# Optimization experiments

Measured on AMD Instinct MI355X. Metric: run time of the kernel, lower is better.

Reference implementation:

```python
import jax, jax.numpy as jnp
import numpy as np

B, C, OUTC, H, W, K, P, S = 4, 64, 64, 128, 128, 3, 1, 1
KK = K * K


def setup_inputs() -> dict:
    key = jax.random.key(0)
    ks = jax.random.split(key, 5)
    x = jax.random.normal(ks[0], (B, C, H, W), dtype=jnp.float32)
    # small-scale offset weights keep learned offsets in a realistic few-pixel range
    w_off = jax.random.normal(ks[1], (2 * KK, C, 3, 3), dtype=jnp.float32) * 0.05
    b_off = jnp.zeros((2 * KK,), dtype=jnp.float32)
    w_mask = jax.random.normal(ks[2], (KK, C, 3, 3), dtype=jnp.float32) * 0.05
    b_mask = jnp.zeros((KK,), dtype=jnp.float32)
    w_dcn = jax.random.normal(ks[3], (OUTC, C, K, K), dtype=jnp.float32) * (1.0 / np.sqrt(C * KK))
    b_dcn = jnp.zeros((OUTC,), dtype=jnp.float32)
    return {"x": x, "w_off": w_off, "b_off": b_off, "w_mask": w_mask,
            "b_mask": b_mask, "w_dcn": w_dcn, "b_dcn": b_dcn}


def _conv3x3(x, w, b):
    y = jax.lax.conv_general_dilated(x, w, (1, 1), ((1, 1), (1, 1)),
                                     dimension_numbers=("NCHW", "OIHW", "NCHW"))
    return y + b[None, :, None, None]


def _deform_conv(x, offset, mask, w, b):
    # torchvision DeformConv2d (v2, modulated). offset layout: [B, kk, (dy,dx), H, W]
    Ho = (H + 2 * P - K) // S + 1
    Wo = (W + 2 * P - K) // S + 1
    off = offset.reshape(B, KK, 2, Ho, Wo)
    dy, dx = off[:, :, 0], off[:, :, 1]                      # [B,kk,Ho,Wo]
    ki, kj = jnp.meshgrid(jnp.arange(K), jnp.arange(K), indexing="ij")
    ki = ki.reshape(KK).astype(jnp.float32)
    kj = kj.reshape(KK).astype(jnp.float32)
    hg = (jnp.arange(Ho) * S - P).astype(jnp.float32)
    wg = (jnp.arange(Wo) * S - P).astype(jnp.float32)
    py = dy + ki[None, :, None, None] + hg[None, None, :, None]   # sample y coord
    px = dx + kj[None, :, None, None] + wg[None, None, None, :]   # sample x coord

    y0f = jnp.floor(py)
    x0f = jnp.floor(px)
    ly = py - y0f
    lx = px - x0f
    y0 = y0f.astype(jnp.int32)
    x0 = x0f.astype(jnp.int32)

    x_flat = x.reshape(B, C, H * W)

    def sample(yi, xi, wgt):
        valid = (yi >= 0) & (yi < H) & (xi >= 0) & (xi < W)
        idx = jnp.clip(yi, 0, H - 1) * W + jnp.clip(xi, 0, W - 1)  # [B,kk,Ho,Wo]
        g = jax.vmap(lambda xb, ib: xb[:, ib])(x_flat, idx)        # [B,C,kk,Ho,Wo]
        return g * (wgt * valid)[:, None]

    acc = (sample(y0, x0, (1 - ly) * (1 - lx))
           + sample(y0, x0 + 1, (1 - ly) * lx)
           + sample(y0 + 1, x0, ly * (1 - lx))
           + sample(y0 + 1, x0 + 1, ly * lx))                      # [B,C,kk,Ho,Wo]
    acc = acc * mask.reshape(B, 1, KK, Ho, Wo)
    out = jnp.einsum("bckhw,ock->bohw", acc, w.reshape(OUTC, C, KK))
    return out + b[None, :, None, None]


def reference(x, w_off, b_off, w_mask, b_mask, w_dcn, b_dcn):
    offset = _conv3x3(x, w_off, b_off)
    mask = jax.nn.sigmoid(_conv3x3(x, w_mask, b_mask))
    out = _deform_conv(x, offset, mask, w_dcn, b_dcn)
    return out, offset
```

## Files before the change

kernel.cpp:

```cpp
#include <hip/hip_runtime.h>
#include <hip/hip_bf16.h>
#include <math.h>

#define BB 4
#define CC 64
#define OCN 64
#define HH 128
#define WW 128
#define HW (HH*WW)
#define KKN 9
#define APAD 200

typedef short short8 __attribute__((ext_vector_type(8)));
typedef short short4v __attribute__((ext_vector_type(4)));
typedef float floatx4 __attribute__((ext_vector_type(4)));
typedef unsigned int uintx4 __attribute__((ext_vector_type(4)));

__device__ __forceinline__ float bf2f_us(unsigned short u) {
    return __uint_as_float(((unsigned)u) << 16);
}
__device__ __forceinline__ short f2bfs(float f) {
    __hip_bfloat16 h = __float2bfloat16(f);
    return *reinterpret_cast<short*>(&h);
}
__device__ __forceinline__ uintx4 as_u4(short8 v) {
    union { short8 s; uintx4 u; } x; x.s = v; return x.u;
}
__device__ __forceinline__ float blo(unsigned d) { return __uint_as_float(d << 16); }
__device__ __forceinline__ float bhi(unsigned d) { return __uint_as_float(d & 0xffff0000u); }

__global__ __launch_bounds__(256) void transpose_prep(
    const float* __restrict__ x,
    const float* __restrict__ w_dcn, const float* __restrict__ w_off,
    const float* __restrict__ b_off, const float* __restrict__ w_mask,
    const float* __restrict__ b_mask,
    __hip_bfloat16* __restrict__ xt, __hip_bfloat16* __restrict__ wTf,
    __hip_bfloat16* __restrict__ wOf, float* __restrict__ rebias)
{
    int blk = blockIdx.x;
    int tid = threadIdx.x;
    if (blk < BB * 512) {
        __shared__ float tile[64][33];
        int pixbase = (blk & 511) * 32;
        int b       = blk >> 9;
        const float* xb = x + (size_t)b * CC * HW;
        int p = tid & 31;
        #pragma unroll
        for (int i = 0; i < 8; ++i) {
            int c = (tid >> 5) * 8 + i;
            tile[c][p] = xb[(size_t)c * HW + pixbase + p];
        }
        __syncthreads();
        __hip_bfloat16* xo = xt + ((size_t)b * HW + pixbase) * CC;
        int pixl = tid >> 3;
        int c8t  = tid & 7;
        short8 o;
        #pragma unroll
        for (int i = 0; i < 8; ++i) o[i] = f2bfs(tile[c8t * 8 + i][pixl]);
        *reinterpret_cast<short8*>(&xo[(size_t)pixl * CC + c8t * 8]) = o;
        return;
    }
    int i = (blk - BB * 512) * 256 + tid;
    if (i < 18 * 4 * 64 * 8) {
        int jj = i & 7;
        int l  = (i >> 3) & 63;
        int nt = (i >> 9) & 3;
        int s  = i >> 11;
        int oc = nt * 16 + (l & 15);
        int kk = s * 32 + ((l >> 4) << 3) + jj;
        int c  = kk & 63;
        int kt = kk >> 6;
        wTf[i] = __float2bfloat16(w_dcn[(oc * CC + c) * 9 + kt]);
    }
    int j = i - 18 * 4 * 64 * 8;
    if (j >= 0 && j < 18 * 2 * 64 * 8) {
        int jj = j & 7;
        int l  = (j >> 3) & 63;
        int nt = (j >> 9) & 1;
        int s  = j >> 10;
        int oc = nt * 16 + (l & 15);
        int kk = s * 32 + ((l >> 4) << 3) + jj;
        int c  = kk & 63;
        int kt = kk >> 6;
        float v = 0.0f;
        if (oc < 18)      v = w_off[(oc * CC + c) * 9 + kt];
        else if (oc < 27) v = w_mask[((oc - 18) * CC + c) * 9 + kt];
        wOf[j] = __float2bfloat16(v);
    }
    int r = j - 18 * 2 * 64 * 8;
    if (r >= 0 && r < 27) rebias[r] = (r < 18) ? b_off[r] : b_mask[r - 18];
}

__global__ __launch_bounds__(256, 4) void deform_fused(
    const __hip_bfloat16* __restrict__ xt,
    const __hip_bfloat16* __restrict__ wTf, const __hip_bfloat16* __restrict__ wOf,
    const float* __restrict__ rebias, const float* __restrict__ b_dcn,
    float* __restrict__ off_out, float* __restrict__ out)
{
    __shared__ __align__(16) __hip_bfloat16 accs[64][APAD];
    __shared__ uintx4 tabs[KKN][64];
    __shared__ __hip_bfloat16 offs_l[18][68];
    __shared__ __hip_bfloat16 ms_l[KKN][68];

    int tid    = threadIdx.x;
    int lane   = tid & 63;
    int wv     = __builtin_amdgcn_readfirstlane(tid >> 6);
    int lane15 = lane & 15;
    int lq     = lane >> 4;
    int nt     = wv & 1;
    int ph     = wv >> 1;
    int pix    = tid >> 3;
    int c8     = tid & 7;
    int co     = c8 * 16;
    int kreg   = lq << 3;

    int wo0 = (blockIdx.x & 1) * 64;
    int row = (blockIdx.x >> 1) & (HH - 1);
    int b   = blockIdx.x >> 8;

    const char* xtb = (const char*)(xt + (size_t)b * HW * CC);
    const short8* wTf8 = (const short8*)wTf;
    const short8* wOf8 = (const short8*)wOf;
    const short8 zero8 = {0,0,0,0,0,0,0,0};

    floatx4 accomA[2] = {{0,0,0,0},{0,0,0,0}};
    for (int chunk = 0; chunk < 3; ++chunk) {
        int y = row + chunk - 1;
        bool yvalid = (unsigned)y < (unsigned)HH;
        int yc = min(max(y, 0), HH - 1);
        short8 v[2][3];
        #pragma unroll
        for (int h = 0; h < 2; ++h) {
            #pragma unroll
            for (int kl = 0; kl < 3; ++kl) {
                int xw = wo0 + h * 32 + pix + kl - 1;
                bool valid = yvalid && ((unsigned)xw < (unsigned)WW);
                int xc = min(max(xw, 0), WW - 1);
                short8 t = *(const short8*)(xtb + (((yc * WW) + xc) << 7) + co);
                v[h][kl] = valid ? t : zero8;
            }
        }
        #pragma unroll
        for (int h = 0; h < 2; ++h)
            #pragma unroll
            for (int kl = 0; kl < 3; ++kl)
                *reinterpret_cast<short8*>(&accs[h * 32 + pix][kl * 64 + c8 * 8]) = v[h][kl];
        __syncthreads();

        #pragma unroll
        for (int step = 0; step < 6; ++step) {
            int s = chunk * 6 + step;
            short8 bfrag = wOf8[(size_t)(s * 2 + nt) * 64 + lane];
            #pragma unroll
            for (int q = 0; q < 2; ++q) {
                int pg = ph * 2 + q;
                short8 a = *reinterpret_cast<const short8*>(&accs[pg * 16 + lane15][step * 32 + kreg]);
                accomA[q] = __builtin_amdgcn_mfma_f32_16x16x32_bf16(a, bfrag, accomA[q], 0, 0, 0);
            }
        }
        __syncthreads();
    }

    #pragma unroll
    for (int q = 0; q < 2; ++q) {
        int pg = ph * 2 + q;
        int pcl = pg * 16 + lq * 4;
        int oc = nt * 16 + lane15;
        if (oc < 18) {
            float bias = rebias[oc];
            floatx4 o = accomA[q];
            o[0] += bias; o[1] += bias; o[2] += bias; o[3] += bias;
            *reinterpret_cast<floatx4*>(
                &off_out[(((size_t)b * 18 + oc) * HH + row) * WW + wo0 + pcl]) = o;
            short4v ob = { f2bfs(o[0]), f2bfs(o[1]), f2bfs(o[2]), f2bfs(o[3]) };
            *reinterpret_cast<short4v*>(&offs_l[oc][pcl]) = ob;
        } else if (oc < 27) {
            float bias = rebias[oc];
            short4v mb;
            #pragma unroll
            for (int t = 0; t < 4; ++t)
                mb[t] = f2bfs(1.0f / (1.0f + expf(-(accomA[q][t] + bias))));
            *reinterpret_cast<short4v*>(&ms_l[oc - 18][pcl]) = mb;
        }
    }
    __syncthreads();

    for (int e = tid; e < KKN * 64; e += 256) {
        int k = e >> 6, p = e & 63;
        float dy = bf2f_us(*(const unsigned short*)&offs_l[2 * k][p]);
        float dx = bf2f_us(*(const unsigned short*)&offs_l[2 * k + 1][p]);
        float m  = bf2f_us(*(const unsigned short*)&ms_l[k][p]);
        float py = dy + (float)(k / 3) + (float)(row - 1);
        float px = dx + (float)(k % 3) + (float)(wo0 + p - 1);
        float y0f = floorf(py), x0f = floorf(px);
        float ly = py - y0f, lx = px - x0f;
        int y0 = (int)y0f, x0 = (int)x0f;
        uintx4 rec;
        #pragma unroll
        for (int t = 0; t < 4; ++t) {
            int yi = y0 + (t >> 1), xi = x0 + (t & 1);
            float wy = (t >> 1) ? ly : 1.0f - ly;
            float wx = (t & 1)  ? lx : 1.0f - lx;
            bool valid = ((unsigned)yi < (unsigned)HH) && ((unsigned)xi < (unsigned)WW);
            int yc2 = min(max(yi, 0), HH - 1);
            int xc2 = min(max(xi, 0), WW - 1);
            __hip_bfloat16 hw = __float2bfloat16(valid ? wy * wx * m : 0.0f);
            unsigned short wb = *reinterpret_cast<unsigned short*>(&hw);
            rec[t] = (unsigned)(yc2 * WW + xc2) | ((unsigned)wb << 16);
        }
        tabs[k][p] = rec;
    }
    __syncthreads();

    short8 buf[2][4];
    uintx4 tb[2];
    floatx4 accv[4] = {{0,0,0,0},{0,0,0,0},{0,0,0,0},{0,0,0,0}};

#define ISSUE(G) do { \
    uintx4 _t = tabs[(G) >> 1][pix + ((G) & 1) * 32]; \
    tb[(G) & 1] = _t; \
    buf[(G) & 1][0] = *(const short8*)(xtb + ((_t[0] & 0xffffu) << 7) + co); \
    buf[(G) & 1][1] = *(const short8*)(xtb + ((_t[1] & 0xffffu) << 7) + co); \
    buf[(G) & 1][2] = *(const short8*)(xtb + ((_t[2] & 0xffffu) << 7) + co); \
    buf[(G) & 1][3] = *(const short8*)(xtb + ((_t[3] & 0xffffu) << 7) + co); \
} while (0)

#define COMBINE(G) do { \
    float fA[8] = {0,0,0,0,0,0,0,0}; \
    _Pragma("unroll") \
    for (int t = 0; t < 4; ++t) { \
        float wt = __uint_as_float(tb[(G) & 1][t] & 0xffff0000u); \
        uintx4 dA = as_u4(buf[(G) & 1][t]); \
        _Pragma("unroll") \
        for (int jq = 0; jq < 4; ++jq) { \
            fA[2 * jq]     = fmaf(wt, blo(dA[jq]), fA[2 * jq]); \
            fA[2 * jq + 1] = fmaf(wt, bhi(dA[jq]), fA[2 * jq + 1]); \
        } \
    } \
    short8 oA; \
    _Pragma("unroll") \
    for (int jq = 0; jq < 8; ++jq) { oA[jq] = f2bfs(fA[jq]); } \
    *reinterpret_cast<short8*>( \
        &accs[((G) & 1) * 32 + pix][(((G) >> 1) % 3) * 64 + c8 * 8]) = oA; \
} while (0)

#define CMFMA(CH) do { \
    _Pragma("unroll") \
    for (int step = 0; step < 6; ++step) { \
        int s = (CH) * 6 + step; \
        short8 bfrag = wTf8[(size_t)(s * 4 + wv) * 64 + lane]; \
        _Pragma("unroll") \
        for (int pg = 0; pg < 4; ++pg) { \
            short8 a = *reinterpret_cast<const short8*>(&accs[pg * 16 + lane15][step * 32 + kreg]); \
            accv[pg] = __builtin_amdgcn_mfma_f32_16x16x32_bf16(a, bfrag, accv[pg], 0, 0, 0); \
        } \
    } \
} while (0)

    ISSUE(0); ISSUE(1);
    COMBINE(0); ISSUE(2);
    COMBINE(1); ISSUE(3);
    COMBINE(2); ISSUE(4);
    COMBINE(3); ISSUE(5);
    COMBINE(4); COMBINE(5);
    __syncthreads();
    ISSUE(6); ISSUE(7);
    CMFMA(0);
    asm volatile("s_waitcnt lgkmcnt(0)" ::: "memory");
    __builtin_amdgcn_s_barrier();
    COMBINE(6); ISSUE(8);
    COMBINE(7); ISSUE(9);
    COMBINE(8); ISSUE(10);
    COMBINE(9); ISSUE(11);
    COMBINE(10); COMBINE(11);
    __syncthreads();
    ISSUE(12); ISSUE(13);
    CMFMA(1);
    asm volatile("s_waitcnt lgkmcnt(0)" ::: "memory");
    __builtin_amdgcn_s_barrier();
    COMBINE(12); ISSUE(14);
    COMBINE(13); ISSUE(15);
    COMBINE(14); ISSUE(16);
    COMBINE(15); ISSUE(17);
    COMBINE(16); COMBINE(17);
    __syncthreads();
    CMFMA(2);

#undef ISSUE
#undef COMBINE
#undef CMFMA

    {
        int oc = wv * 16 + lane15;
        float bias = b_dcn[oc];
        #pragma unroll
        for (int pg = 0; pg < 4; ++pg) {
            int pcol = wo0 + pg * 16 + lq * 4;
            floatx4 o = accv[pg];
            o[0] += bias; o[1] += bias; o[2] += bias; o[3] += bias;
            *reinterpret_cast<floatx4*>(&out[(((size_t)b * OCN + oc) * HH + row) * WW + pcol]) = o;
        }
    }
}

extern "C" void kernel_launch(void* const* d_in, const int* in_sizes, int n_in,
                              void* d_out, int out_size, void* d_ws, size_t ws_size,
                              hipStream_t stream) {
    const float* x      = (const float*)d_in[0];
    const float* w_off  = (const float*)d_in[1];
    const float* b_off  = (const float*)d_in[2];
    const float* w_mask = (const float*)d_in[3];
    const float* b_mask = (const float*)d_in[4];
    const float* w_dcn  = (const float*)d_in[5];
    const float* b_dcn  = (const float*)d_in[6];

    float* out     = (float*)d_out;
    float* off_out = out + (size_t)BB * OCN * HW;

    float* rebias  = (float*)d_ws;
    __hip_bfloat16* xt  = (__hip_bfloat16*)(rebias + 32);
    __hip_bfloat16* wTf = xt + (size_t)BB * HW * CC;
    __hip_bfloat16* wOf = wTf + 18 * 4 * 64 * 8;

    int prep_total  = 18 * 4 * 64 * 8 + 18 * 2 * 64 * 8 + 27;
    int prep_blocks = (prep_total + 255) / 256;
    transpose_prep<<<BB * 512 + prep_blocks, 256, 0, stream>>>(
        x, w_dcn, w_off, b_off, w_mask, b_mask, xt, wTf, wOf, rebias);

    deform_fused<<<BB * HH * 2, 256, 0, stream>>>(
        xt, wTf, wOf, rebias, b_dcn, off_out, out);
}
```

Baseline: 39.96 us.

## Overhaul transpose, offset-conv loads, gather pipelining and block order in deform kernel

The transpose prep kernel now handles 64 pixels per block, reading with float4 loads into an XOR-swizzled shared tile so the transposed reads avoid bank conflicts. The offset/mask conv loads its MFMA A fragments straight from global memory into registers, which removes the LDS staging and two barriers per row chunk. The deformable gather pipeline goes from double to triple buffering so three gathers are in flight before each combine, and the combine uses packed float2 FMAs. Block indices are swizzled so neighbouring blocks land on different rows, which may change cache locality. The cost is more registers, which could reduce occupancy, and redundant global loads in the offset conv.

```diff
diff --git a/kernel.cpp b/kernel.cpp
--- a/kernel.cpp
+++ b/kernel.cpp
@@ -14,6 +14,7 @@
 typedef short short8 __attribute__((ext_vector_type(8)));
 typedef short short4v __attribute__((ext_vector_type(4)));
 typedef float floatx4 __attribute__((ext_vector_type(4)));
+typedef float floatx2 __attribute__((ext_vector_type(2)));
 typedef unsigned int uintx4 __attribute__((ext_vector_type(4)));
 
 __device__ __forceinline__ float bf2f_us(unsigned short u) {
@@ -39,28 +40,34 @@
 {
     int blk = blockIdx.x;
     int tid = threadIdx.x;
-    if (blk < BB * 512) {
-        __shared__ float tile[64][33];
-        int pixbase = (blk & 511) * 32;
-        int b       = blk >> 9;
+    if (blk < BB * 256) {
+        __shared__ float tile[64][64];
+        int pixbase = (blk & 255) * 64;
+        int b       = blk >> 8;
         const float* xb = x + (size_t)b * CC * HW;
-        int p = tid & 31;
-        #pragma unroll
-        for (int i = 0; i < 8; ++i) {
-            int c = (tid >> 5) * 8 + i;
-            tile[c][p] = xb[(size_t)c * HW + pixbase + p];
+        #pragma unroll
+        for (int i = 0; i < 4; ++i) {
+            int c  = (tid >> 4) + i * 16;
+            int p4 = (tid & 15) * 4;
+            floatx4 v = *reinterpret_cast<const floatx4*>(xb + (size_t)c * HW + pixbase + p4);
+            int cs = p4 ^ (((c >> 3) & 7) << 2);
+            *reinterpret_cast<floatx4*>(&tile[c][cs]) = v;
         }
         __syncthreads();
         __hip_bfloat16* xo = xt + ((size_t)b * HW + pixbase) * CC;
-        int pixl = tid >> 3;
-        int c8t  = tid & 7;
-        short8 o;
-        #pragma unroll
-        for (int i = 0; i < 8; ++i) o[i] = f2bfs(tile[c8t * 8 + i][pixl]);
-        *reinterpret_cast<short8*>(&xo[(size_t)pixl * CC + c8t * 8]) = o;
+        int c8t = tid & 7;
+        #pragma unroll
+        for (int i = 0; i < 2; ++i) {
+            int pixl = (tid >> 3) + i * 32;
+            short8 o;
+            #pragma unroll
+            for (int j = 0; j < 8; ++j)
+                o[j] = f2bfs(tile[c8t * 8 + j][pixl ^ (c8t << 2)]);
+            *reinterpret_cast<short8*>(&xo[(size_t)pixl * CC + c8t * 8]) = o;
+        }
         return;
     }
-    int i = (blk - BB * 512) * 256 + tid;
+    int i = (blk - BB * 256) * 256 + tid;
     if (i < 18 * 4 * 64 * 8) {
         int jj = i & 7;
         int l  = (i >> 3) & 63;
@@ -97,7 +104,7 @@
     const float* __restrict__ rebias, const float* __restrict__ b_dcn,
     float* __restrict__ off_out, float* __restrict__ out)
 {
-    __shared__ __align__(16) __hip_bfloat16 accs[64][APAD];
+    __shared__ __align__(16) char scr[64 * APAD * 2];
     __shared__ uintx4 tabs[KKN][64];
     __shared__ __hip_bfloat16 offs_l[18][68];
     __shared__ __hip_bfloat16 ms_l[KKN][68];
@@ -114,9 +121,11 @@
     int co     = c8 * 16;
     int kreg   = lq << 3;
 
-    int wo0 = (blockIdx.x & 1) * 64;
-    int row = (blockIdx.x >> 1) & (HH - 1);
-    int b   = blockIdx.x >> 8;
+    int bid = blockIdx.x;
+    int swz = ((bid & 7) << 7) | (bid >> 3);
+    int wo0 = (swz & 1) * 64;
+    int row = (swz >> 1) & (HH - 1);
+    int b   = swz >> 8;
 
     const char* xtb = (const char*)(xt + (size_t)b * HW * CC);
     const short8* wTf8 = (const short8*)wTf;
@@ -124,41 +133,33 @@
     const short8 zero8 = {0,0,0,0,0,0,0,0};
 
     floatx4 accomA[2] = {{0,0,0,0},{0,0,0,0}};
-    for (int chunk = 0; chunk < 3; ++chunk) {
-        int y = row + chunk - 1;
-        bool yvalid = (unsigned)y < (unsigned)HH;
+    #pragma unroll
+    for (int ky = 0; ky < 3; ++ky) {
+        int y = row + ky - 1;
+        bool yv = (unsigned)y < (unsigned)HH;
         int yc = min(max(y, 0), HH - 1);
-        short8 v[2][3];
-        #pragma unroll
-        for (int h = 0; h < 2; ++h) {
-            #pragma unroll
-            for (int kl = 0; kl < 3; ++kl) {
-                int xw = wo0 + h * 32 + pix + kl - 1;
-                bool valid = yvalid && ((unsigned)xw < (unsigned)WW);
-                int xc = min(max(xw, 0), WW - 1);
-                short8 t = *(const short8*)(xtb + (((yc * WW) + xc) << 7) + co);
-                v[h][kl] = valid ? t : zero8;
-            }
-        }
-        #pragma unroll
-        for (int h = 0; h < 2; ++h)
-            #pragma unroll
-            for (int kl = 0; kl < 3; ++kl)
-                *reinterpret_cast<short8*>(&accs[h * 32 + pix][kl * 64 + c8 * 8]) = v[h][kl];
-        __syncthreads();
-
-        #pragma unroll
-        for (int step = 0; step < 6; ++step) {
-            int s = chunk * 6 + step;
-            short8 bfrag = wOf8[(size_t)(s * 2 + nt) * 64 + lane];
+        short8 af[2][6];
+        #pragma unroll
+        for (int s6 = 0; s6 < 6; ++s6) {
+            int kx = s6 >> 1;
+            int colb = (s6 & 1) * 64 + lq * 16;
             #pragma unroll
             for (int q = 0; q < 2; ++q) {
                 int pg = ph * 2 + q;
-                short8 a = *reinterpret_cast<const short8*>(&accs[pg * 16 + lane15][step * 32 + kreg]);
-                accomA[q] = __builtin_amdgcn_mfma_f32_16x16x32_bf16(a, bfrag, accomA[q], 0, 0, 0);
+                int xw = wo0 + pg * 16 + lane15 + kx - 1;
+                bool v = yv && ((unsigned)xw < (unsigned)WW);
+                int xc = min(max(xw, 0), WW - 1);
+                short8 t = *(const short8*)(xtb + (((yc * WW) + xc) << 7) + colb);
+                af[q][s6] = v ? t : zero8;
             }
         }
-        __syncthreads();
+        #pragma unroll
+        for (int s6 = 0; s6 < 6; ++s6) {
+            int s = ky * 6 + s6;
+            short8 bfrag = wOf8[(size_t)(s * 2 + nt) * 64 + lane];
+            accomA[0] = __builtin_amdgcn_mfma_f32_16x16x32_bf16(af[0][s6], bfrag, accomA[0], 0, 0, 0);
+            accomA[1] = __builtin_amdgcn_mfma_f32_16x16x32_bf16(af[1][s6], bfrag, accomA[1], 0, 0, 0);
+        }
     }
 
     #pragma unroll
@@ -212,36 +213,41 @@
     }
     __syncthreads();
 
-    short8 buf[2][4];
-    uintx4 tb[2];
+    short8 buf[3][4];
+    uintx4 tb[3];
     floatx4 accv[4] = {{0,0,0,0},{0,0,0,0},{0,0,0,0},{0,0,0,0}};
+
+#define ACCS(PIX, COLB) (scr + (PIX) * (APAD * 2) + (COLB))
 
 #define ISSUE(G) do { \
     uintx4 _t = tabs[(G) >> 1][pix + ((G) & 1) * 32]; \
-    tb[(G) & 1] = _t; \
-    buf[(G) & 1][0] = *(const short8*)(xtb + ((_t[0] & 0xffffu) << 7) + co); \
-    buf[(G) & 1][1] = *(const short8*)(xtb + ((_t[1] & 0xffffu) << 7) + co); \
-    buf[(G) & 1][2] = *(const short8*)(xtb + ((_t[2] & 0xffffu) << 7) + co); \
-    buf[(G) & 1][3] = *(const short8*)(xtb + ((_t[3] & 0xffffu) << 7) + co); \
+    tb[(G) % 3] = _t; \
+    buf[(G) % 3][0] = *(const short8*)(xtb + ((_t[0] & 0xffffu) << 7) + co); \
+    buf[(G) % 3][1] = *(const short8*)(xtb + ((_t[1] & 0xffffu) << 7) + co); \
+    buf[(G) % 3][2] = *(const short8*)(xtb + ((_t[2] & 0xffffu) << 7) + co); \
+    buf[(G) % 3][3] = *(const short8*)(xtb + ((_t[3] & 0xffffu) << 7) + co); \
 } while (0)
 
 #define COMBINE(G) do { \
-    float fA[8] = {0,0,0,0,0,0,0,0}; \
+    floatx2 f2[4] = {{0,0},{0,0},{0,0},{0,0}}; \
     _Pragma("unroll") \
     for (int t = 0; t < 4; ++t) { \
-        float wt = __uint_as_float(tb[(G) & 1][t] & 0xffff0000u); \
-        uintx4 dA = as_u4(buf[(G) & 1][t]); \
+        float wt = __uint_as_float(tb[(G) % 3][t] & 0xffff0000u); \
+        floatx2 wt2 = {wt, wt}; \
+        uintx4 dA = as_u4(buf[(G) % 3][t]); \
         _Pragma("unroll") \
         for (int jq = 0; jq < 4; ++jq) { \
-            fA[2 * jq]     = fmaf(wt, blo(dA[jq]), fA[2 * jq]); \
-            fA[2 * jq + 1] = fmaf(wt, bhi(dA[jq]), fA[2 * jq + 1]); \
+            floatx2 xv = { blo(dA[jq]), bhi(dA[jq]) }; \
+            f2[jq] = __builtin_elementwise_fma(wt2, xv, f2[jq]); \
         } \
     } \
     short8 oA; \
     _Pragma("unroll") \
-    for (int jq = 0; jq < 8; ++jq) { oA[jq] = f2bfs(fA[jq]); } \
-    *reinterpret_cast<short8*>( \
-        &accs[((G) & 1) * 32 + pix][(((G) >> 1) % 3) * 64 + c8 * 8]) = oA; \
+    for (int jq = 0; jq < 4; ++jq) { \
+        oA[2 * jq]     = f2bfs(f2[jq][0]); \
+        oA[2 * jq + 1] = f2bfs(f2[jq][1]); \
+    } \
+    *(short8*)ACCS(((G) & 1) * 32 + pix, (((G) >> 1) % 3) * 128 + c8 * 16) = oA; \
 } while (0)
 
 #define CMFMA(CH) do { \
@@ -251,44 +257,44 @@
         short8 bfrag = wTf8[(size_t)(s * 4 + wv) * 64 + lane]; \
         _Pragma("unroll") \
         for (int pg = 0; pg < 4; ++pg) { \
-            short8 a = *reinterpret_cast<const short8*>(&accs[pg * 16 + lane15][step * 32 + kreg]); \
+            short8 a = *(const short8*)ACCS(pg * 16 + lane15, step * 64 + kreg * 2); \
             accv[pg] = __builtin_amdgcn_mfma_f32_16x16x32_bf16(a, bfrag, accv[pg], 0, 0, 0); \
         } \
     } \
 } while (0)
 
-    ISSUE(0); ISSUE(1);
-    COMBINE(0); ISSUE(2);
-    COMBINE(1); ISSUE(3);
-    COMBINE(2); ISSUE(4);
-    COMBINE(3); ISSUE(5);
-    COMBINE(4); COMBINE(5);
-    __syncthreads();
-    ISSUE(6); ISSUE(7);
+    ISSUE(0); ISSUE(1); ISSUE(2);
+    COMBINE(0); ISSUE(3);
+    COMBINE(1); ISSUE(4);
+    COMBINE(2); ISSUE(5);
+    COMBINE(3); ISSUE(6);
+    COMBINE(4); ISSUE(7);
+    COMBINE(5); ISSUE(8);
+    __syncthreads();
     CMFMA(0);
     asm volatile("s_waitcnt lgkmcnt(0)" ::: "memory");
     __builtin_amdgcn_s_barrier();
-    COMBINE(6); ISSUE(8);
-    COMBINE(7); ISSUE(9);
-    COMBINE(8); ISSUE(10);
-    COMBINE(9); ISSUE(11);
-    COMBINE(10); COMBINE(11);
-    __syncthreads();
-    ISSUE(12); ISSUE(13);
+    COMBINE(6); ISSUE(9);
+    COMBINE(7); ISSUE(10);
+    COMBINE(8); ISSUE(11);
+    COMBINE(9); ISSUE(12);
+    COMBINE(10); ISSUE(13);
+    COMBINE(11); ISSUE(14);
+    __syncthreads();
     CMFMA(1);
     asm volatile("s_waitcnt lgkmcnt(0)" ::: "memory");
     __builtin_amdgcn_s_barrier();
-    COMBINE(12); ISSUE(14);
-    COMBINE(13); ISSUE(15);
-    COMBINE(14); ISSUE(16);
-    COMBINE(15); ISSUE(17);
-    COMBINE(16); COMBINE(17);
+    COMBINE(12); ISSUE(15);
+    COMBINE(13); ISSUE(16);
+    COMBINE(14); ISSUE(17);
+    COMBINE(15); COMBINE(16); COMBINE(17);
     __syncthreads();
     CMFMA(2);
 
 #undef ISSUE
 #undef COMBINE
 #undef CMFMA
+#undef ACCS
 
     {
         int oc = wv * 16 + lane15;
@@ -324,7 +330,7 @@
 
     int prep_total  = 18 * 4 * 64 * 8 + 18 * 2 * 64 * 8 + 27;
     int prep_blocks = (prep_total + 255) / 256;
-    transpose_prep<<<BB * 512 + prep_blocks, 256, 0, stream>>>(
+    transpose_prep<<<BB * 256 + prep_blocks, 256, 0, stream>>>(
         x, w_dcn, w_off, b_off, w_mask, b_mask, xt, wTf, wOf, rebias);
 
     deform_fused<<<BB * HH * 2, 256, 0, stream>>>(
```

Result: slower. 50.93 us (+27.4%).
